# Kernel optimization log

Measured on AMD Instinct MI355X. Metric: run time of the kernel, lower is better.

The kernel has to match this reference:

```python
import jax, jax.numpy as jnp
import numpy as np

GS = 7          # grid size
NB = 2          # boxes per cell
NC = 20         # classes
LAMBDA_COORD = 0.5
LAMBDA_NOOBJ = 0.5


def setup_inputs() -> dict:
    key = jax.random.key(0)
    k1, k2, k3 = jax.random.split(key, 3)
    B = 8192
    C = 5 * NB + NC  # 30
    inputs = jax.random.uniform(k1, (B, GS, GS, C), minval=0.05, maxval=0.95, dtype=jnp.float32)
    targets = jax.random.uniform(k2, (B, GS, GS, C), minval=0.05, maxval=0.95, dtype=jnp.float32)
    obj = jax.random.bernoulli(k3, 0.15, (B, GS, GS)).astype(jnp.float32)
    # _transform_targets writes the SAME box into both box slots and sets conf=1 for obj cells
    targets = targets.at[..., 5:9].set(targets[..., 0:4])
    targets = targets.at[..., 4].set(obj)
    targets = targets.at[..., 9].set(obj)
    return {"inputs": inputs, "targets": targets}


def _yolo_loss(inputs, targets):
    bs = inputs.shape[0]
    gs = inputs.shape[2]
    dt = inputs.dtype

    conf_t = targets[..., 4]
    coord = (conf_t > 0).astype(dt)          # [B,S,S] cells containing an object
    noobj = (conf_t == 0).astype(dt)          # [B,S,S]

    # ---- no-object confidence loss: channels 4 + 5*b for each box b ----
    conf_idx = jnp.arange(NB) * 5 + 4         # [4, 9]
    pc = inputs[..., conf_idx]                # [B,S,S,NB]
    tc = targets[..., conf_idx]
    loss_noobj = jnp.sum(noobj[..., None] * (pc - tc) ** 2)

    # ---- per-cell box matching (vectorizes the pairwise IoU loop) ----
    bp = inputs[..., :5 * NB].reshape(inputs.shape[:3] + (NB, 5))    # [B,S,S,NB,5]
    # original takes boxes_targets[i] (first box of the pair; both slots are identical)
    bt = targets[..., :5 * NB].reshape(targets.shape[:3] + (NB, 5))[..., 0, :]  # [B,S,S,5]

    def to_xyxy(b):
        # faithful to original: xy scaled by 1/gs, wh NOT scaled
        xy = b[..., :2] / gs
        wh = b[..., 2:4]
        return jnp.concatenate([xy - 0.5 * wh, xy + 0.5 * wh], axis=-1)

    pxy = to_xyxy(bp)                          # [B,S,S,NB,4]
    txy = to_xyxy(bt)[..., None, :]            # [B,S,S,1,4]
    lt = jnp.maximum(pxy[..., :2], txy[..., :2])
    rb = jnp.minimum(pxy[..., 2:], txy[..., 2:])
    whi = jnp.clip(rb - lt, 0.0)
    inter = whi[..., 0] * whi[..., 1]          # [B,S,S,NB]
    area = lambda x: (x[..., 2] - x[..., 0]) * (x[..., 3] - x[..., 1])
    iou = inter / (area(pxy) + area(txy) - inter)   # [B,S,S,NB]

    max_iou = jnp.max(iou, axis=-1)            # [B,S,S]
    idx = jnp.argmax(iou, axis=-1)             # [B,S,S] responsible box (first max, like torch)
    idx_b = jnp.broadcast_to(idx[..., None, None], idx.shape + (1, 5))
    rp = jnp.take_along_axis(bp, idx_b, axis=-2)[..., 0, :]  # [B,S,S,5] responsible preds

    loss_xy = jnp.sum(coord[..., None] * (rp[..., :2] - bt[..., :2]) ** 2)
    loss_wh = jnp.sum(coord[..., None] * (jnp.sqrt(rp[..., 2:4]) - jnp.sqrt(bt[..., 2:4])) ** 2)
    loss_obj = jnp.sum(coord * (rp[..., 4] - max_iou) ** 2)
    loss_class = jnp.sum(coord[..., None] * (inputs[..., 5 * NB:] - targets[..., 5 * NB:]) ** 2)

    loss_boxes = LAMBDA_COORD * (loss_xy + loss_wh) / bs
    loss_conf = (loss_obj + LAMBDA_NOOBJ * loss_noobj) / bs
    loss_class = loss_class / bs
    return loss_boxes, loss_conf, loss_class


def reference(inputs, targets):
    return _yolo_loss(inputs, targets)
```

## Files before the change

### kernel.cpp

```cpp
#include <hip/hip_runtime.h>

#define GS 7
#define CC 30

__device__ __forceinline__ void cell_losses(const float* __restrict__ f,
                                            const float* __restrict__ t,
                                            float& o_boxes, float& o_conf, float& o_cls) {
    const float inv_gs = 0.14285714285714285f;

    const float conf_t = t[4];
    const float coord  = (conf_t > 0.0f)  ? 1.0f : 0.0f;
    const float noobj  = (conf_t == 0.0f) ? 1.0f : 0.0f;

    const float d0 = f[4] - t[4];
    const float d1 = f[9] - t[9];
    const float l_noobj = noobj * (d0 * d0 + d1 * d1);

    const float bt0 = t[0], bt1 = t[1], bt2 = t[2], bt3 = t[3];
    const float ttx = bt0 * inv_gs, tty = bt1 * inv_gs;
    const float txmin = ttx - 0.5f * bt2, tymin = tty - 0.5f * bt3;
    const float txmax = ttx + 0.5f * bt2, tymax = tty + 0.5f * bt3;
    const float tarea = (txmax - txmin) * (tymax - tymin);

    const float px0 = f[0], py0 = f[1], pw0 = f[2], ph0 = f[3], pc0 = f[4];
    const float px1 = f[5], py1 = f[6], pw1 = f[7], ph1 = f[8], pc1 = f[9];

    float iou0, iou1;
    {
        const float cx = px0 * inv_gs, cy = py0 * inv_gs;
        const float xmin = cx - 0.5f * pw0, ymin = cy - 0.5f * ph0;
        const float xmax = cx + 0.5f * pw0, ymax = cy + 0.5f * ph0;
        const float wx = fmaxf(fminf(xmax, txmax) - fmaxf(xmin, txmin), 0.0f);
        const float wy = fmaxf(fminf(ymax, tymax) - fmaxf(ymin, tymin), 0.0f);
        const float inter = wx * wy;
        const float parea = (xmax - xmin) * (ymax - ymin);
        iou0 = inter / (parea + tarea - inter);
    }
    {
        const float cx = px1 * inv_gs, cy = py1 * inv_gs;
        const float xmin = cx - 0.5f * pw1, ymin = cy - 0.5f * ph1;
        const float xmax = cx + 0.5f * pw1, ymax = cy + 0.5f * ph1;
        const float wx = fmaxf(fminf(xmax, txmax) - fmaxf(xmin, txmin), 0.0f);
        const float wy = fmaxf(fminf(ymax, tymax) - fmaxf(ymin, tymin), 0.0f);
        const float inter = wx * wy;
        const float parea = (xmax - xmin) * (ymax - ymin);
        iou1 = inter / (parea + tarea - inter);
    }
    const bool  sel1    = iou1 > iou0;
    const float max_iou = fmaxf(iou0, iou1);

    const float rp0 = sel1 ? px1 : px0;
    const float rp1 = sel1 ? py1 : py0;
    const float rp2 = sel1 ? pw1 : pw0;
    const float rp3 = sel1 ? ph1 : ph0;
    const float rp4 = sel1 ? pc1 : pc0;

    const float dx = rp0 - bt0, dy = rp1 - bt1;
    const float sw = sqrtf(rp2) - sqrtf(bt2);
    const float sh = sqrtf(rp3) - sqrtf(bt3);
    const float dob = rp4 - max_iou;
    const float l_box = dx * dx + dy * dy + sw * sw + sh * sh;
    const float l_obj = dob * dob;

    float l_cls = 0.0f;
    #pragma unroll
    for (int j = 10; j < 30; ++j) {
        const float d = f[j] - t[j];
        l_cls += d * d;
    }

    o_boxes += coord * l_box;
    o_conf  += coord * l_obj + 0.5f * l_noobj;
    o_cls   += coord * l_cls;
}

__global__ __launch_bounds__(256) void yolo_main(
        const float* __restrict__ in,
        const float* __restrict__ tg,
        float* __restrict__ ws,
        int npairs, int ncells, int pstride) {
    const int pair = blockIdx.x * 256 + threadIdx.x;

    float a_boxes = 0.0f, a_conf = 0.0f, a_class = 0.0f;

    if (pair < npairs) {
        const float4* gin = (const float4*)(in + (size_t)pair * (2 * CC));
        const float4* gtg = (const float4*)(tg + (size_t)pair * (2 * CC));

        float fi[60], ft[60];
        float4* vi = (float4*)fi;
        float4* vt = (float4*)ft;
        #pragma unroll
        for (int k = 0; k < 15; ++k) vi[k] = gin[k];
        #pragma unroll
        for (int k = 0; k < 15; ++k) vt[k] = gtg[k];

        cell_losses(fi,      ft,      a_boxes, a_conf, a_class);
        cell_losses(fi + 30, ft + 30, a_boxes, a_conf, a_class);
    }
    if ((ncells & 1) && pair == npairs) {
        const size_t c = (size_t)(ncells - 1) * CC;
        cell_losses(in + c, tg + c, a_boxes, a_conf, a_class);
    }

    #pragma unroll
    for (int off = 32; off > 0; off >>= 1) {
        a_boxes += __shfl_down(a_boxes, off, 64);
        a_conf  += __shfl_down(a_conf,  off, 64);
        a_class += __shfl_down(a_class, off, 64);
    }
    __shared__ float s_red[4][3];
    const int wave = threadIdx.x >> 6;
    if ((threadIdx.x & 63) == 0) {
        s_red[wave][0] = a_boxes;
        s_red[wave][1] = a_conf;
        s_red[wave][2] = a_class;
    }
    __syncthreads();
    if (threadIdx.x == 0) {
        const float b = s_red[0][0] + s_red[1][0] + s_red[2][0] + s_red[3][0];
        const float c = s_red[0][1] + s_red[1][1] + s_red[2][1] + s_red[3][1];
        const float k = s_red[0][2] + s_red[1][2] + s_red[2][2] + s_red[3][2];
        ws[blockIdx.x]               = b;
        ws[blockIdx.x + pstride]     = c;
        ws[blockIdx.x + 2 * pstride] = k;
    }
}

__global__ __launch_bounds__(256) void yolo_finalize(
        const float* __restrict__ ws, float* __restrict__ out,
        int nblocks, int pstride, float inv_bs) {
    float b = 0.0f, c = 0.0f, k = 0.0f;
    for (int i = threadIdx.x; i < nblocks; i += 256) {
        b += ws[i];
        c += ws[i + pstride];
        k += ws[i + 2 * pstride];
    }
    #pragma unroll
    for (int off = 32; off > 0; off >>= 1) {
        b += __shfl_down(b, off, 64);
        c += __shfl_down(c, off, 64);
        k += __shfl_down(k, off, 64);
    }
    __shared__ float s_red[4][3];
    const int wave = threadIdx.x >> 6;
    if ((threadIdx.x & 63) == 0) {
        s_red[wave][0] = b;
        s_red[wave][1] = c;
        s_red[wave][2] = k;
    }
    __syncthreads();
    if (threadIdx.x == 0) {
        const float tb = s_red[0][0] + s_red[1][0] + s_red[2][0] + s_red[3][0];
        const float tc = s_red[0][1] + s_red[1][1] + s_red[2][1] + s_red[3][1];
        const float tk = s_red[0][2] + s_red[1][2] + s_red[2][2] + s_red[3][2];
        out[0] = 0.5f * tb * inv_bs;
        out[1] = tc * inv_bs;
        out[2] = tk * inv_bs;
    }
}

extern "C" void kernel_launch(void* const* d_in, const int* in_sizes, int n_in,
                              void* d_out, int out_size, void* d_ws, size_t ws_size,
                              hipStream_t stream) {
    const float* in = (const float*)d_in[0];
    const float* tg = (const float*)d_in[1];
    float* out = (float*)d_out;
    float* ws  = (float*)d_ws;

    const int ncells = in_sizes[0] / CC;
    const int B = ncells / (GS * GS);
    const float inv_bs = 1.0f / (float)B;

    const int npairs  = ncells / 2;
    const int nblocks = (npairs + 255) / 256;
    const int pstride = nblocks;

    yolo_main<<<nblocks, 256, 0, stream>>>(in, tg, ws, npairs, ncells, pstride);
    yolo_finalize<<<1, 256, 0, stream>>>(ws, out, nblocks, pstride, inv_bs);
}
```

Before: 138.0 us.

## Stage cells through LDS with coalesced float4 loads, one cell per thread

Replaces the per-thread strided float4 loads of two cells into registers with a cooperative, coalesced block load of 256 cells of inputs and targets into shared memory, after which each thread processes one cell from LDS. This targets the uncoalesced global access pattern, where each lane read a 240-byte contiguous chunk. In exchange it uses about 60 KB of LDS per block, which limits occupancy, adds a barrier, and doubles the block count. Reads from LDS at a 30-float stride may also cause some bank conflicts.

```diff
diff --git a/kernel.cpp b/kernel.cpp
--- a/kernel.cpp
+++ b/kernel.cpp
@@ -2,105 +2,114 @@
 
 #define GS 7
 #define CC 30
-
-__device__ __forceinline__ void cell_losses(const float* __restrict__ f,
-                                            const float* __restrict__ t,
-                                            float& o_boxes, float& o_conf, float& o_cls) {
-    const float inv_gs = 0.14285714285714285f;
-
-    const float conf_t = t[4];
-    const float coord  = (conf_t > 0.0f)  ? 1.0f : 0.0f;
-    const float noobj  = (conf_t == 0.0f) ? 1.0f : 0.0f;
-
-    const float d0 = f[4] - t[4];
-    const float d1 = f[9] - t[9];
-    const float l_noobj = noobj * (d0 * d0 + d1 * d1);
-
-    const float bt0 = t[0], bt1 = t[1], bt2 = t[2], bt3 = t[3];
-    const float ttx = bt0 * inv_gs, tty = bt1 * inv_gs;
-    const float txmin = ttx - 0.5f * bt2, tymin = tty - 0.5f * bt3;
-    const float txmax = ttx + 0.5f * bt2, tymax = tty + 0.5f * bt3;
-    const float tarea = (txmax - txmin) * (tymax - tymin);
-
-    const float px0 = f[0], py0 = f[1], pw0 = f[2], ph0 = f[3], pc0 = f[4];
-    const float px1 = f[5], py1 = f[6], pw1 = f[7], ph1 = f[8], pc1 = f[9];
-
-    float iou0, iou1;
-    {
-        const float cx = px0 * inv_gs, cy = py0 * inv_gs;
-        const float xmin = cx - 0.5f * pw0, ymin = cy - 0.5f * ph0;
-        const float xmax = cx + 0.5f * pw0, ymax = cy + 0.5f * ph0;
-        const float wx = fmaxf(fminf(xmax, txmax) - fmaxf(xmin, txmin), 0.0f);
-        const float wy = fmaxf(fminf(ymax, tymax) - fmaxf(ymin, tymin), 0.0f);
-        const float inter = wx * wy;
-        const float parea = (xmax - xmin) * (ymax - ymin);
-        iou0 = inter / (parea + tarea - inter);
-    }
-    {
-        const float cx = px1 * inv_gs, cy = py1 * inv_gs;
-        const float xmin = cx - 0.5f * pw1, ymin = cy - 0.5f * ph1;
-        const float xmax = cx + 0.5f * pw1, ymax = cy + 0.5f * ph1;
-        const float wx = fmaxf(fminf(xmax, txmax) - fmaxf(xmin, txmin), 0.0f);
-        const float wy = fmaxf(fminf(ymax, tymax) - fmaxf(ymin, tymin), 0.0f);
-        const float inter = wx * wy;
-        const float parea = (xmax - xmin) * (ymax - ymin);
-        iou1 = inter / (parea + tarea - inter);
-    }
-    const bool  sel1    = iou1 > iou0;
-    const float max_iou = fmaxf(iou0, iou1);
-
-    const float rp0 = sel1 ? px1 : px0;
-    const float rp1 = sel1 ? py1 : py0;
-    const float rp2 = sel1 ? pw1 : pw0;
-    const float rp3 = sel1 ? ph1 : ph0;
-    const float rp4 = sel1 ? pc1 : pc0;
-
-    const float dx = rp0 - bt0, dy = rp1 - bt1;
-    const float sw = sqrtf(rp2) - sqrtf(bt2);
-    const float sh = sqrtf(rp3) - sqrtf(bt3);
-    const float dob = rp4 - max_iou;
-    const float l_box = dx * dx + dy * dy + sw * sw + sh * sh;
-    const float l_obj = dob * dob;
-
-    float l_cls = 0.0f;
-    #pragma unroll
-    for (int j = 10; j < 30; ++j) {
-        const float d = f[j] - t[j];
-        l_cls += d * d;
-    }
-
-    o_boxes += coord * l_box;
-    o_conf  += coord * l_obj + 0.5f * l_noobj;
-    o_cls   += coord * l_cls;
-}
+#define CPB 256
 
 __global__ __launch_bounds__(256) void yolo_main(
         const float* __restrict__ in,
         const float* __restrict__ tg,
         float* __restrict__ ws,
-        int npairs, int ncells, int pstride) {
-    const int pair = blockIdx.x * 256 + threadIdx.x;
+        int ncells, int pstride) {
+    __shared__ float s_in[CPB * CC];
+    __shared__ float s_tg[CPB * CC];
+    __shared__ float s_red[4][3];
+
+    const int tid  = threadIdx.x;
+    const int base = blockIdx.x * CPB;
+    int n = ncells - base;
+    if (n > CPB) n = CPB;
+
+    if (n == CPB) {
+        const float4* gin = (const float4*)(in + (size_t)base * CC);
+        const float4* gtg = (const float4*)(tg + (size_t)base * CC);
+        float4* lin = (float4*)s_in;
+        float4* ltg = (float4*)s_tg;
+        #pragma unroll
+        for (int k = 0; k < 8; ++k) {
+            const int idx = tid + k * 256;
+            if (idx < 1920) {
+                lin[idx] = gin[idx];
+                ltg[idx] = gtg[idx];
+            }
+        }
+    } else {
+        const int lim = n * CC;
+        for (int k = tid; k < lim; k += 256) {
+            s_in[k] = in[(size_t)base * CC + k];
+            s_tg[k] = tg[(size_t)base * CC + k];
+        }
+    }
+    __syncthreads();
 
     float a_boxes = 0.0f, a_conf = 0.0f, a_class = 0.0f;
+    if (tid < n) {
+        const float* f = s_in + tid * CC;
+        const float* t = s_tg + tid * CC;
+        const float inv_gs = 0.14285714285714285f;
 
-    if (pair < npairs) {
-        const float4* gin = (const float4*)(in + (size_t)pair * (2 * CC));
-        const float4* gtg = (const float4*)(tg + (size_t)pair * (2 * CC));
+        const float conf_t = t[4];
+        const float coord  = (conf_t > 0.0f)  ? 1.0f : 0.0f;
+        const float noobj  = (conf_t == 0.0f) ? 1.0f : 0.0f;
 
-        float fi[60], ft[60];
-        float4* vi = (float4*)fi;
-        float4* vt = (float4*)ft;
+        const float d0 = f[4] - t[4];
+        const float d1 = f[9] - t[9];
+        const float l_noobj = noobj * (d0 * d0 + d1 * d1);
+
+        const float bt0 = t[0], bt1 = t[1], bt2 = t[2], bt3 = t[3];
+        const float ttx = bt0 * inv_gs, tty = bt1 * inv_gs;
+        const float txmin = ttx - 0.5f * bt2, tymin = tty - 0.5f * bt3;
+        const float txmax = ttx + 0.5f * bt2, tymax = tty + 0.5f * bt3;
+        const float tarea = (txmax - txmin) * (tymax - tymin);
+
+        const float px0 = f[0], py0 = f[1], pw0 = f[2], ph0 = f[3], pc0 = f[4];
+        const float px1 = f[5], py1 = f[6], pw1 = f[7], ph1 = f[8], pc1 = f[9];
+
+        float iou0, iou1;
+        {
+            const float cx = px0 * inv_gs, cy = py0 * inv_gs;
+            const float xmin = cx - 0.5f * pw0, ymin = cy - 0.5f * ph0;
+            const float xmax = cx + 0.5f * pw0, ymax = cy + 0.5f * ph0;
+            const float wx = fmaxf(fminf(xmax, txmax) - fmaxf(xmin, txmin), 0.0f);
+            const float wy = fmaxf(fminf(ymax, tymax) - fmaxf(ymin, tymin), 0.0f);
+            const float inter = wx * wy;
+            const float parea = (xmax - xmin) * (ymax - ymin);
+            iou0 = inter / (parea + tarea - inter);
+        }
+        {
+            const float cx = px1 * inv_gs, cy = py1 * inv_gs;
+            const float xmin = cx - 0.5f * pw1, ymin = cy - 0.5f * ph1;
+            const float xmax = cx + 0.5f * pw1, ymax = cy + 0.5f * ph1;
+            const float wx = fmaxf(fminf(xmax, txmax) - fmaxf(xmin, txmin), 0.0f);
+            const float wy = fmaxf(fminf(ymax, tymax) - fmaxf(ymin, tymin), 0.0f);
+            const float inter = wx * wy;
+            const float parea = (xmax - xmin) * (ymax - ymin);
+            iou1 = inter / (parea + tarea - inter);
+        }
+        const bool  sel1    = iou1 > iou0;
+        const float max_iou = fmaxf(iou0, iou1);
+
+        const float rp0 = sel1 ? px1 : px0;
+        const float rp1 = sel1 ? py1 : py0;
+        const float rp2 = sel1 ? pw1 : pw0;
+        const float rp3 = sel1 ? ph1 : ph0;
+        const float rp4 = sel1 ? pc1 : pc0;
+
+        const float dx = rp0 - bt0, dy = rp1 - bt1;
+        const float sw = sqrtf(rp2) - sqrtf(bt2);
+        const float sh = sqrtf(rp3) - sqrtf(bt3);
+        const float dob = rp4 - max_iou;
+        const float l_box = dx * dx + dy * dy + sw * sw + sh * sh;
+        const float l_obj = dob * dob;
+
+        float l_cls = 0.0f;
         #pragma unroll
-        for (int k = 0; k < 15; ++k) vi[k] = gin[k];
-        #pragma unroll
-        for (int k = 0; k < 15; ++k) vt[k] = gtg[k];
+        for (int j = 10; j < 30; ++j) {
+            const float d = f[j] - t[j];
+            l_cls += d * d;
+        }
 
-        cell_losses(fi,      ft,      a_boxes, a_conf, a_class);
-        cell_losses(fi + 30, ft + 30, a_boxes, a_conf, a_class);
-    }
-    if ((ncells & 1) && pair == npairs) {
-        const size_t c = (size_t)(ncells - 1) * CC;
-        cell_losses(in + c, tg + c, a_boxes, a_conf, a_class);
+        a_boxes = coord * l_box;
+        a_conf  = coord * l_obj + 0.5f * l_noobj;
+        a_class = coord * l_cls;
     }
 
     #pragma unroll
@@ -109,15 +118,14 @@
         a_conf  += __shfl_down(a_conf,  off, 64);
         a_class += __shfl_down(a_class, off, 64);
     }
-    __shared__ float s_red[4][3];
-    const int wave = threadIdx.x >> 6;
-    if ((threadIdx.x & 63) == 0) {
+    const int wave = tid >> 6;
+    if ((tid & 63) == 0) {
         s_red[wave][0] = a_boxes;
         s_red[wave][1] = a_conf;
         s_red[wave][2] = a_class;
     }
     __syncthreads();
-    if (threadIdx.x == 0) {
+    if (tid == 0) {
         const float b = s_red[0][0] + s_red[1][0] + s_red[2][0] + s_red[3][0];
         const float c = s_red[0][1] + s_red[1][1] + s_red[2][1] + s_red[3][1];
         const float k = s_red[0][2] + s_red[1][2] + s_red[2][2] + s_red[3][2];
@@ -172,10 +180,9 @@
     const int B = ncells / (GS * GS);
     const float inv_bs = 1.0f / (float)B;
 
-    const int npairs  = ncells / 2;
-    const int nblocks = (npairs + 255) / 256;
+    const int nblocks = (ncells + CPB - 1) / CPB;
     const int pstride = nblocks;
 
-    yolo_main<<<nblocks, 256, 0, stream>>>(in, tg, ws, npairs, ncells, pstride);
+    yolo_main<<<nblocks, 256, 0, stream>>>(in, tg, ws, ncells, pstride);
     yolo_finalize<<<1, 256, 0, stream>>>(ws, out, nblocks, pstride, inv_bs);
 }
```

New measurement: 117.5 us. 1.17x faster.

## Stage cell tiles through LDS with coalesced loads in grid-stride persistent waves

Applied to the files above, without the earlier changes.

Each wave now loads a tile of 64 cells (1920 floats) per input with lane-contiguous float4 loads into shared memory, then each lane reads its cell from LDS. This replaces the old per-thread strided 240-byte float4 loads, which coalesced poorly. The launch uses a fixed 512-block grid where each wave loops over tiles and writes its own partial sums, so the block-level reduction is dropped. The cost is 61KB of LDS per block, which limits occupancy, and strided LDS reads at a stride of 30 floats that may cause bank conflicts.

```diff
diff --git a/kernel.cpp b/kernel.cpp
--- a/kernel.cpp
+++ b/kernel.cpp
@@ -1,106 +1,133 @@
 #include <hip/hip_runtime.h>
 
-#define GS 7
 #define CC 30
-
-__device__ __forceinline__ void cell_losses(const float* __restrict__ f,
-                                            const float* __restrict__ t,
-                                            float& o_boxes, float& o_conf, float& o_cls) {
-    const float inv_gs = 0.14285714285714285f;
-
-    const float conf_t = t[4];
-    const float coord  = (conf_t > 0.0f)  ? 1.0f : 0.0f;
-    const float noobj  = (conf_t == 0.0f) ? 1.0f : 0.0f;
-
-    const float d0 = f[4] - t[4];
-    const float d1 = f[9] - t[9];
-    const float l_noobj = noobj * (d0 * d0 + d1 * d1);
-
-    const float bt0 = t[0], bt1 = t[1], bt2 = t[2], bt3 = t[3];
-    const float ttx = bt0 * inv_gs, tty = bt1 * inv_gs;
-    const float txmin = ttx - 0.5f * bt2, tymin = tty - 0.5f * bt3;
-    const float txmax = ttx + 0.5f * bt2, tymax = tty + 0.5f * bt3;
-    const float tarea = (txmax - txmin) * (tymax - tymin);
-
-    const float px0 = f[0], py0 = f[1], pw0 = f[2], ph0 = f[3], pc0 = f[4];
-    const float px1 = f[5], py1 = f[6], pw1 = f[7], ph1 = f[8], pc1 = f[9];
-
-    float iou0, iou1;
-    {
-        const float cx = px0 * inv_gs, cy = py0 * inv_gs;
-        const float xmin = cx - 0.5f * pw0, ymin = cy - 0.5f * ph0;
-        const float xmax = cx + 0.5f * pw0, ymax = cy + 0.5f * ph0;
-        const float wx = fmaxf(fminf(xmax, txmax) - fmaxf(xmin, txmin), 0.0f);
-        const float wy = fmaxf(fminf(ymax, tymax) - fmaxf(ymin, tymin), 0.0f);
-        const float inter = wx * wy;
-        const float parea = (xmax - xmin) * (ymax - ymin);
-        iou0 = inter / (parea + tarea - inter);
-    }
-    {
-        const float cx = px1 * inv_gs, cy = py1 * inv_gs;
-        const float xmin = cx - 0.5f * pw1, ymin = cy - 0.5f * ph1;
-        const float xmax = cx + 0.5f * pw1, ymax = cy + 0.5f * ph1;
-        const float wx = fmaxf(fminf(xmax, txmax) - fmaxf(xmin, txmin), 0.0f);
-        const float wy = fmaxf(fminf(ymax, tymax) - fmaxf(ymin, tymin), 0.0f);
-        const float inter = wx * wy;
-        const float parea = (xmax - xmin) * (ymax - ymin);
-        iou1 = inter / (parea + tarea - inter);
-    }
-    const bool  sel1    = iou1 > iou0;
-    const float max_iou = fmaxf(iou0, iou1);
-
-    const float rp0 = sel1 ? px1 : px0;
-    const float rp1 = sel1 ? py1 : py0;
-    const float rp2 = sel1 ? pw1 : pw0;
-    const float rp3 = sel1 ? ph1 : ph0;
-    const float rp4 = sel1 ? pc1 : pc0;
-
-    const float dx = rp0 - bt0, dy = rp1 - bt1;
-    const float sw = sqrtf(rp2) - sqrtf(bt2);
-    const float sh = sqrtf(rp3) - sqrtf(bt3);
-    const float dob = rp4 - max_iou;
-    const float l_box = dx * dx + dy * dy + sw * sw + sh * sh;
-    const float l_obj = dob * dob;
-
-    float l_cls = 0.0f;
-    #pragma unroll
-    for (int j = 10; j < 30; ++j) {
-        const float d = f[j] - t[j];
-        l_cls += d * d;
-    }
-
-    o_boxes += coord * l_box;
-    o_conf  += coord * l_obj + 0.5f * l_noobj;
-    o_cls   += coord * l_cls;
-}
+#define TPW 64
+#define WPB 4
+#define TILE_FLOATS (TPW * CC)
+#define TILE_VEC4   (TILE_FLOATS / 4)
 
 __global__ __launch_bounds__(256) void yolo_main(
         const float* __restrict__ in,
         const float* __restrict__ tg,
         float* __restrict__ ws,
-        int npairs, int ncells, int pstride) {
-    const int pair = blockIdx.x * 256 + threadIdx.x;
+        int ncells, int nwaves_total, int pstride) {
+    __shared__ float s_in[WPB * TILE_FLOATS];
+    __shared__ float s_tg[WPB * TILE_FLOATS];
+
+    const int tid   = threadIdx.x;
+    const int lane  = tid & 63;
+    const int wave  = tid >> 6;
+    const int gwave = blockIdx.x * WPB + wave;
+
+    float* lin = s_in + wave * TILE_FLOATS;
+    float* ltg = s_tg + wave * TILE_FLOATS;
+
+    const int ntiles = (ncells + TPW - 1) / TPW;
+    const float inv_gs = 0.14285714285714285f;
 
     float a_boxes = 0.0f, a_conf = 0.0f, a_class = 0.0f;
 
-    if (pair < npairs) {
-        const float4* gin = (const float4*)(in + (size_t)pair * (2 * CC));
-        const float4* gtg = (const float4*)(tg + (size_t)pair * (2 * CC));
+    for (int tile = gwave; tile < ntiles; tile += nwaves_total) {
+        const int cbase = tile * TPW;
+        int n = ncells - cbase;
+        if (n > TPW) n = TPW;
 
-        float fi[60], ft[60];
-        float4* vi = (float4*)fi;
-        float4* vt = (float4*)ft;
-        #pragma unroll
-        for (int k = 0; k < 15; ++k) vi[k] = gin[k];
-        #pragma unroll
-        for (int k = 0; k < 15; ++k) vt[k] = gtg[k];
+        if (n == TPW) {
+            const float4* gin = (const float4*)(in + (size_t)cbase * CC);
+            const float4* gtg = (const float4*)(tg + (size_t)cbase * CC);
+            float4* vin = (float4*)lin;
+            float4* vtg = (float4*)ltg;
+            float4 bi[8], bt[8];
+            #pragma unroll
+            for (int k = 0; k < 8; ++k) {
+                const int idx = k * 64 + lane;
+                if (idx < TILE_VEC4) { bi[k] = gin[idx]; bt[k] = gtg[idx]; }
+            }
+            #pragma unroll
+            for (int k = 0; k < 8; ++k) {
+                const int idx = k * 64 + lane;
+                if (idx < TILE_VEC4) { vin[idx] = bi[k]; vtg[idx] = bt[k]; }
+            }
+        } else {
+            const int lim = n * CC;
+            for (int k = lane; k < lim; k += 64) {
+                lin[k] = in[(size_t)cbase * CC + k];
+                ltg[k] = tg[(size_t)cbase * CC + k];
+            }
+        }
+        asm volatile("s_waitcnt vmcnt(0) lgkmcnt(0)" ::: "memory");
+        __builtin_amdgcn_wave_barrier();
 
-        cell_losses(fi,      ft,      a_boxes, a_conf, a_class);
-        cell_losses(fi + 30, ft + 30, a_boxes, a_conf, a_class);
-    }
-    if ((ncells & 1) && pair == npairs) {
-        const size_t c = (size_t)(ncells - 1) * CC;
-        cell_losses(in + c, tg + c, a_boxes, a_conf, a_class);
+        if (lane < n) {
+            const float* f = lin + lane * CC;
+            const float* t = ltg + lane * CC;
+
+            const float conf_t = t[4];
+            const float coord  = (conf_t > 0.0f)  ? 1.0f : 0.0f;
+            const float noobj  = (conf_t == 0.0f) ? 1.0f : 0.0f;
+
+            const float d0 = f[4] - t[4];
+            const float d1 = f[9] - t[9];
+            const float l_noobj = noobj * (d0 * d0 + d1 * d1);
+
+            const float bt0 = t[0], bt1 = t[1], bt2 = t[2], bt3 = t[3];
+            const float ttx = bt0 * inv_gs, tty = bt1 * inv_gs;
+            const float txmin = ttx - 0.5f * bt2, tymin = tty - 0.5f * bt3;
+            const float txmax = ttx + 0.5f * bt2, tymax = tty + 0.5f * bt3;
+            const float tarea = (txmax - txmin) * (tymax - tymin);
+
+            const float px0 = f[0], py0 = f[1], pw0 = f[2], ph0 = f[3], pc0 = f[4];
+            const float px1 = f[5], py1 = f[6], pw1 = f[7], ph1 = f[8], pc1 = f[9];
+
+            float iou0, iou1;
+            {
+                const float cx = px0 * inv_gs, cy = py0 * inv_gs;
+                const float xmin = cx - 0.5f * pw0, ymin = cy - 0.5f * ph0;
+                const float xmax = cx + 0.5f * pw0, ymax = cy + 0.5f * ph0;
+                const float wx = fmaxf(fminf(xmax, txmax) - fmaxf(xmin, txmin), 0.0f);
+                const float wy = fmaxf(fminf(ymax, tymax) - fmaxf(ymin, tymin), 0.0f);
+                const float inter = wx * wy;
+                const float parea = (xmax - xmin) * (ymax - ymin);
+                iou0 = inter / (parea + tarea - inter);
+            }
+            {
+                const float cx = px1 * inv_gs, cy = py1 * inv_gs;
+                const float xmin = cx - 0.5f * pw1, ymin = cy - 0.5f * ph1;
+                const float xmax = cx + 0.5f * pw1, ymax = cy + 0.5f * ph1;
+                const float wx = fmaxf(fminf(xmax, txmax) - fmaxf(xmin, txmin), 0.0f);
+                const float wy = fmaxf(fminf(ymax, tymax) - fmaxf(ymin, tymin), 0.0f);
+                const float inter = wx * wy;
+                const float parea = (xmax - xmin) * (ymax - ymin);
+                iou1 = inter / (parea + tarea - inter);
+            }
+            const bool  sel1    = iou1 > iou0;
+            const float max_iou = fmaxf(iou0, iou1);
+
+            const float rp0 = sel1 ? px1 : px0;
+            const float rp1 = sel1 ? py1 : py0;
+            const float rp2 = sel1 ? pw1 : pw0;
+            const float rp3 = sel1 ? ph1 : ph0;
+            const float rp4 = sel1 ? pc1 : pc0;
+
+            const float dx = rp0 - bt0, dy = rp1 - bt1;
+            const float sw = sqrtf(rp2) - sqrtf(bt2);
+            const float sh = sqrtf(rp3) - sqrtf(bt3);
+            const float dob = rp4 - max_iou;
+            const float l_box = dx * dx + dy * dy + sw * sw + sh * sh;
+            const float l_obj = dob * dob;
+
+            float l_cls = 0.0f;
+            #pragma unroll
+            for (int j = 10; j < 30; ++j) {
+                const float d = f[j] - t[j];
+                l_cls += d * d;
+            }
+
+            a_boxes += coord * l_box;
+            a_conf  += coord * l_obj + 0.5f * l_noobj;
+            a_class += coord * l_cls;
+        }
+        __builtin_amdgcn_wave_barrier();
     }
 
     #pragma unroll
@@ -109,29 +136,18 @@
         a_conf  += __shfl_down(a_conf,  off, 64);
         a_class += __shfl_down(a_class, off, 64);
     }
-    __shared__ float s_red[4][3];
-    const int wave = threadIdx.x >> 6;
-    if ((threadIdx.x & 63) == 0) {
-        s_red[wave][0] = a_boxes;
-        s_red[wave][1] = a_conf;
-        s_red[wave][2] = a_class;
-    }
-    __syncthreads();
-    if (threadIdx.x == 0) {
-        const float b = s_red[0][0] + s_red[1][0] + s_red[2][0] + s_red[3][0];
-        const float c = s_red[0][1] + s_red[1][1] + s_red[2][1] + s_red[3][1];
-        const float k = s_red[0][2] + s_red[1][2] + s_red[2][2] + s_red[3][2];
-        ws[blockIdx.x]               = b;
-        ws[blockIdx.x + pstride]     = c;
-        ws[blockIdx.x + 2 * pstride] = k;
+    if (lane == 0) {
+        ws[gwave]               = a_boxes;
+        ws[gwave + pstride]     = a_conf;
+        ws[gwave + 2 * pstride] = a_class;
     }
 }
 
 __global__ __launch_bounds__(256) void yolo_finalize(
         const float* __restrict__ ws, float* __restrict__ out,
-        int nblocks, int pstride, float inv_bs) {
+        int nparts, int pstride, float inv_bs) {
     float b = 0.0f, c = 0.0f, k = 0.0f;
-    for (int i = threadIdx.x; i < nblocks; i += 256) {
+    for (int i = threadIdx.x; i < nparts; i += 256) {
         b += ws[i];
         c += ws[i + pstride];
         k += ws[i + 2 * pstride];
@@ -169,13 +185,13 @@
     float* ws  = (float*)d_ws;
 
     const int ncells = in_sizes[0] / CC;
-    const int B = ncells / (GS * GS);
+    const int B = ncells / (49);
     const float inv_bs = 1.0f / (float)B;
 
-    const int npairs  = ncells / 2;
-    const int nblocks = (npairs + 255) / 256;
-    const int pstride = nblocks;
+    const int nblocks = 512;
+    const int nwaves  = nblocks * WPB;
+    const int pstride = nwaves;
 
-    yolo_main<<<nblocks, 256, 0, stream>>>(in, tg, ws, npairs, ncells, pstride);
-    yolo_finalize<<<1, 256, 0, stream>>>(ws, out, nblocks, pstride, inv_bs);
+    yolo_main<<<nblocks, 256, 0, stream>>>(in, tg, ws, ncells, nwaves, pstride);
+    yolo_finalize<<<1, 256, 0, stream>>>(ws, out, nwaves, pstride, inv_bs);
 }
```

Result: faster. 115.3 us (-16.5%).
